# Optimization experiments

Hardware: AMD Instinct MI355X
Metric: run time of the kernel (lower is better)

The kernel has to match this reference:

```python
import jax, jax.numpy as jnp
import numpy as np

D, R, C = 4, 6, 32
P = 2 * R + 1          # 13 (both pixel patch and memory patch, since memory_patch_R == R)
N = P * P              # 169
DIL_INT = 15


def corr_sampler(f1, f2, p, dil):
    """SpatialCorrelationSampler(kernel_size=1, patch_size=p, dilation_patch=dil).
    out[b,i,j,y,x] = sum_c f1[b,c,y,x] * f2[b,c, y+(i-Rp)*dil, x+(j-Rp)*dil] (zero pad)."""
    Rp = (p - 1) // 2
    pad = Rp * dil
    b, c, h, w = f1.shape
    f2p = jnp.pad(f2, ((0, 0), (0, 0), (pad, pad), (pad, pad)))
    outs = [jnp.einsum('bchw,bchw->bhw', f1, f2p[:, :, i * dil:i * dil + h, j * dil:j * dil + w])
            for i in range(p) for j in range(p)]
    return jnp.stack(outs, 1).reshape(b, p, p, h, w)


def bilinear_gather(im, ys, xs):
    """Bilinear sample im [b,c,H,W] at float coords ys,xs [b,N,h,w]; zeros outside."""
    H, W = im.shape[2], im.shape[3]
    y0 = jnp.floor(ys)
    x0 = jnp.floor(xs)
    wy = ys - y0
    wx = xs - x0

    def g(yi, xi):
        valid = ((yi >= 0) & (yi < H) & (xi >= 0) & (xi < W)).astype(im.dtype)
        yc = jnp.clip(yi, 0, H - 1).astype(jnp.int32)
        xc = jnp.clip(xi, 0, W - 1).astype(jnp.int32)
        out = jax.vmap(lambda imb, yb, xb: imb[:, yb, xb])(im, yc, xc)  # [b,c,N,h,w]
        return out * valid[:, None]

    return (g(y0, x0) * ((1 - wy) * (1 - wx))[:, None]
            + g(y0, x0 + 1) * ((1 - wy) * wx)[:, None]
            + g(y0 + 1, x0) * (wy * (1 - wx))[:, None]
            + g(y0 + 1, x0 + 1) * (wy * wx)[:, None])


def deform_im2col(im, offset, p):
    """Deformable im2col: for each output pixel (y,x) and kernel pos (ky,kx),
    bilinearly sample im at (y+ky-Rp+off_y, x+kx-Rp+off_x). offset [...,0]=x, [...,1]=y.
    Returns [b,c,p*p,h,w]."""
    b, c, h, w = im.shape
    Rp = (p - 1) // 2
    ky, kx = jnp.meshgrid(jnp.arange(p) - Rp, jnp.arange(p) - Rp, indexing='ij')
    ky = ky.reshape(-1).astype(im.dtype)
    kx = kx.reshape(-1).astype(im.dtype)
    ys = (jnp.arange(h, dtype=im.dtype)[None, None, :, None]
          + ky[None, :, None, None] + offset[..., 1][:, None])  # [b,N,h,w]
    xs = (jnp.arange(w, dtype=im.dtype)[None, None, None, :]
          + kx[None, :, None, None] + offset[..., 0][:, None])
    return bilinear_gather(im, ys, xs)


def unfold_patches(x, p, pad):
    """F.unfold(kernel_size=p, padding=pad) -> [b,c,p*p,h,w]."""
    b, c, h, w = x.shape
    xp = jnp.pad(x, ((0, 0), (0, 0), (pad, pad), (pad, pad)))
    cols = [xp[:, :, i:i + h, j:j + w] for i in range(p) for j in range(p)]
    return jnp.stack(cols, 2)


def _forward(feats_r, feats_t, quantized_r, ref_index, current_ind):
    ri = np.asarray(ref_index)
    ci = int(current_ind)
    diffs = [ci - int(x) for x in ri]
    nsearch = sum(1 for d in diffs if d > DIL_INT)
    dirates = [min(4, d // DIL_INT + 1) for d in diffs if d > DIL_INT]
    nref = feats_r.shape[0]
    b, c, h, w = feats_t.shape

    # offset grid: _y,_x = meshgrid(ij) so grid[...,0]=x-offset, grid[...,1]=y-offset
    _y, _x = jnp.meshgrid(jnp.arange(-R, R + 1), jnp.arange(-R, R + 1), indexing='ij')
    grid = jnp.stack([_x, _y], -1).astype(feats_t.dtype)  # [P,P,2]

    corrs_pixel = []
    offset0 = []
    for s in range(nsearch):
        cc = corr_sampler(feats_t, feats_r[s], P, dirates[s])             # [b,P,P,h,w]
        soft = jax.nn.softmax(cc.reshape(b, N, h * w), axis=1).reshape(b, P, P, h, w)
        off = jnp.einsum('bijhw,ijd->bhwd', soft, grid) * dirates[s]      # [b,h,w,2]
        offset0.append(off)
        col0 = deform_im2col(feats_r[s], off, P)                          # [b,c,N,h,w]
        corrs_pixel.append(jnp.einsum('bchw,bcnhw->bnhw', feats_t, col0).reshape(b, N, h * w))
    for ind in range(nsearch, nref):
        corrs_pixel.append(corr_sampler(feats_t, feats_r[ind], P, 1).reshape(b, N, h * w))

    corr_pixel = jax.nn.softmax(jnp.concatenate(corrs_pixel, 1), axis=1)  # [b,nref*N,h*w]

    # prep: float + stride-D subsampling (C-channel input, so no one-hot branch)
    qr = [quantized_r[i][:, :, ::D, ::D] for i in range(nref)]            # [b,C,h,w]
    cols = [deform_im2col(qr[i], offset0[i], P).reshape(b, C, N, h * w) for i in range(nsearch)]
    cols += [unfold_patches(qr[i], P, R).reshape(b, C, N, h * w) for i in range(nsearch, nref)]
    image_uf = jnp.concatenate(cols, 2)                                   # [b,C,nref*N,h*w]

    out = jnp.einsum('bkl,bckl->bcl', corr_pixel, image_uf).reshape(b, C, h, w)
    return out


def setup_inputs() -> dict:
    key = jax.random.key(0)
    k1, k2, k3 = jax.random.split(key, 3)
    feats_r = jax.random.normal(k1, (3, 1, 64, 56, 56), jnp.float32) * 0.2
    feats_t = jax.random.normal(k2, (1, 64, 56, 56), jnp.float32) * 0.2
    quantized_r = jax.random.uniform(k3, (3, 1, 32, 224, 224), jnp.float32)
    return {
        'feats_r': feats_r,
        'feats_t': feats_t,
        'quantized_r': quantized_r,
        'ref_index': np.array([0, 30, 39], dtype=np.int64),
        'current_ind': 40,
    }


def reference(feats_r, feats_t, quantized_r, ref_index, current_ind):
    return _forward(feats_r, feats_t, quantized_r, ref_index, current_ind)
```

## Files before the change

kernel.cpp:

```cpp
#include <hip/hip_runtime.h>

#define HW    56
#define NPIX  3136
#define CH    64
#define CQ    32
#define PS    13
#define NPOS  169
#define GS    14
#define NG    196
#define G1    15
#define NG1   225

typedef __attribute__((ext_vector_type(8))) short short8;
typedef __attribute__((ext_vector_type(8))) ushort ushort8;
typedef __attribute__((ext_vector_type(4))) float f32x4;

__device__ inline ushort f2bf(float f) {
  unsigned u = __float_as_uint(f);
  return (ushort)((u + 0x7fffu + ((u >> 16) & 1u)) >> 16);
}
__device__ inline float bf2f(ushort u) {
  return __uint_as_float((unsigned)u << 16);
}
__device__ inline void wave_sync() {
  asm volatile("s_waitcnt lgkmcnt(0)" ::: "memory");
  __builtin_amdgcn_sched_barrier(0);
}

__global__ __launch_bounds__(256) void prep_all(
    const float* __restrict__ ft_in,
    const float* __restrict__ fr_in,
    const float* __restrict__ q_in,
    ushort* __restrict__ ft_out,
    ushort* __restrict__ fr_out,
    ushort* __restrict__ qout,
    float* __restrict__ zrow) {
  __shared__ float smem[CQ * (HW + 1)];
  int bid = blockIdx.x, tid = threadIdx.x;
  if (bid < 784) {
    if (bid == 0 && tid < 64) zrow[tid] = 0.f;
    int m = bid / 196, t = bid - m * 196;
    int row0 = (t / 98) * 32;
    int col0 = (t - (t / 98) * 98) * 32;
    const float* src = (m == 0) ? ft_in : fr_in + (size_t)(m - 1) * CH * NPIX;
    ushort* dst      = (m == 0) ? ft_out : fr_out + (size_t)(m - 1) * NPIX * CH;
    int ty = tid >> 3, tx4 = (tid & 7) * 4;
    f32x4 v = *(const f32x4*)&src[(size_t)(row0 + ty) * NPIX + col0 + tx4];
    *(f32x4*)&smem[ty * 33 + tx4] = v;
    __syncthreads();
    int px = tid >> 3, c4 = (tid & 7) * 4;
    ushort4 o;
    o.x = f2bf(smem[(c4 + 0) * 33 + px]);
    o.y = f2bf(smem[(c4 + 1) * 33 + px]);
    o.z = f2bf(smem[(c4 + 2) * 33 + px]);
    o.w = f2bf(smem[(c4 + 3) * 33 + px]);
    *(ushort4*)&dst[(size_t)(col0 + px) * CH + row0 + c4] = o;
  } else {
    int q = bid - 784;
    int r = q / HW, yy = q - r * HW;
    for (int idx = tid; idx < CQ * HW; idx += 256) {
      int c = idx / HW, xx = idx - c * HW;
      smem[c * (HW + 1) + xx] = q_in[((size_t)(r * CQ + c) * 224 + yy * 4) * 224 + xx * 4];
    }
    __syncthreads();
    for (int idx = tid; idx < CQ * HW; idx += 256) {
      int xx = idx >> 5, c = idx & 31;
      qout[(size_t)r * NPIX * CQ + (size_t)(yy * HW + xx) * CQ + c] = f2bf(smem[c * (HW + 1) + xx]);
    }
  }
}

__global__ __launch_bounds__(256, 4) void colorizer_main(
    const ushort* __restrict__ ftb,
    const ushort* __restrict__ frb,
    const ushort* __restrict__ qrb,
    const ushort* __restrict__ zrow,
    float* __restrict__ out)
{
  __shared__ float C1[1024];
  __shared__ float C2[1024];
  __shared__ int   pw[4 * 832];
  __shared__ float Sas[4];
  __shared__ float fqr0[128];
  __shared__ float red2[512];

  int tid = threadIdx.x;
  int wid = tid >> 6, lane = tid & 63;
  int mrow = lane & 15, klane = lane >> 4;

  int bx = blockIdx.x % 28, by = blockIdx.x / 28;
  int Y0 = by * 2, X0 = bx * 2;
  int dy = wid >> 1, dx = wid & 1;
  int y = Y0 + dy, x = X0 + dx;
  int pix = y * HW + x;

  int*   wb   = pw + wid * 832;
  float* e    = (float*)wb;
  float* D    = (float*)(wb + 176);
  float* wg   = (float*)(wb + 384);
  int*   offg = wb + 608;
  float* cc   = (float*)offg;

  if (lane < 16) offg[208 + lane] = -1;

  const ushort* frb0 = frb;
  const ushort* frb1 = frb + (size_t)NPIX * CH;
  const ushort* frb2 = frb + (size_t)2 * NPIX * CH;
  const ushort* qr0b = qrb;
  const ushort* qr1b = qrb + (size_t)NPIX * CQ;
  const ushort* qr2b = qrb + (size_t)2 * NPIX * CQ;

  const ushort* fb = ftb + (size_t)pix * CH;
  const ushort* plo = (mrow == 0) ? (fb + klane * 8) : zrow;
  const ushort* phi = (mrow == 0) ? (fb + 32 + klane * 8) : zrow;
  short8 b_lo = *(const short8*)plo;
  short8 b_hi = *(const short8*)phi;

  const ushort* fb4 = (mrow < 4)
      ? (ftb + (size_t)((Y0 + (mrow >> 1)) * HW + X0 + (mrow & 1)) * CH)
      : zrow;
  short8 b4_lo = *(const short8*)(fb4 + klane * 8);
  short8 b4_hi = *(const short8*)(fb4 + 32 + klane * 8);

#pragma unroll
  for (int k = 0; k < 8; ++k) {
    int j = wid + 4 * k;
    if (j < 30) {
      int r = (j >= 15);
      int t = j - r * 15;
      int g = t * 16 + mrow;
      int gy = g / G1, gx = g - gy * G1;
      int sy = Y0 - 6 + gy, sx = X0 - 6 + gx;
      bool v = (g < NG1) && ((unsigned)sy < HW) && ((unsigned)sx < HW);
      const ushort* base = r ? frb2 : frb1;
      const ushort* rb = v ? (base + (size_t)(sy * HW + sx) * CH) : zrow;
      short8 alo = *(const short8*)(rb + klane * 8);
      short8 ahi = *(const short8*)(rb + 32 + klane * 8);
      f32x4 acc = {0.f, 0.f, 0.f, 0.f};
      acc = __builtin_amdgcn_mfma_f32_16x16x32_bf16(alo, b4_lo, acc, 0, 0, 0);
      acc = __builtin_amdgcn_mfma_f32_16x16x32_bf16(ahi, b4_hi, acc, 0, 0, 0);
      int col = lane & 15;
      if (col < 4) {
        float* Cd = r ? C2 : C1;
        int row0 = t * 16 + (lane >> 4) * 4;
#pragma unroll
        for (int q = 0; q < 4; ++q) Cd[(row0 + q) * 4 + col] = acc[q];
      }
    }
  }
  __syncthreads();

#pragma unroll
  for (int g = 0; g < 11; ++g) {
    int d = g * 16 + mrow;
    int ii = d / PS, jj = d - ii * PS;
    int sy = y + (ii - 6) * 3, sx = x + (jj - 6) * 3;
    bool v = (d < NPOS) && ((unsigned)sy < HW) && ((unsigned)sx < HW);
    const ushort* rb = v ? (frb0 + (size_t)(sy * HW + sx) * CH) : zrow;
    short8 alo = *(const short8*)(rb + klane * 8);
    short8 ahi = *(const short8*)(rb + 32 + klane * 8);
    f32x4 acc = {0.f, 0.f, 0.f, 0.f};
    acc = __builtin_amdgcn_mfma_f32_16x16x32_bf16(alo, b_lo, acc, 0, 0, 0);
    acc = __builtin_amdgcn_mfma_f32_16x16x32_bf16(ahi, b_hi, acc, 0, 0, 0);
    if (mrow == 0) *(f32x4*)&cc[g * 16 + klane * 4] = acc;
  }
  wave_sync();

  float se = 0.f, sxe = 0.f, sye = 0.f;
#pragma unroll
  for (int k = 0; k < 3; ++k) {
    int id = lane + 64 * k;
    if (id < NPOS) {
      float ex = __expf(cc[id]);
      int pi = id / PS, pj = id - (id / PS) * PS;
      se += ex;
      sxe += ex * (float)(pj - 6);
      sye += ex * (float)(pi - 6);
    }
  }
#pragma unroll
  for (int o = 1; o < 64; o <<= 1) {
    se  += __shfl_xor(se, o);
    sxe += __shfl_xor(sxe, o);
    sye += __shfl_xor(sye, o);
  }
  float offx = 3.f * sxe / se;
  float offy = 3.f * sye / se;

  float fy0 = floorf(offy), fx0 = floorf(offx);
  int   iy0 = (int)fy0,     ix0 = (int)fx0;
  float wyf = offy - fy0,   wxf = offx - fx0;
  float w00 = (1.f - wyf) * (1.f - wxf), w01 = (1.f - wyf) * wxf;
  float w10 = wyf * (1.f - wxf),         w11 = wyf * wxf;

#pragma unroll
  for (int g = 0; g < 13; ++g) {
    int d = g * 16 + mrow;
    int a = d / GS, bq = d - a * GS;
    int sy = y + iy0 + a - 6, sx = x + ix0 + bq - 6;
    bool vA = (d < NG) && ((unsigned)sy < HW) && ((unsigned)sx < HW);
    int roA = sy * HW + sx;
    const ushort* rbA = vA ? (frb0 + (size_t)roA * CH) : zrow;
    short8 aAlo = *(const short8*)(rbA + klane * 8);
    short8 aAhi = *(const short8*)(rbA + 32 + klane * 8);
    f32x4 accA = {0.f, 0.f, 0.f, 0.f};
    accA = __builtin_amdgcn_mfma_f32_16x16x32_bf16(aAlo, b_lo, accA, 0, 0, 0);
    accA = __builtin_amdgcn_mfma_f32_16x16x32_bf16(aAhi, b_hi, accA, 0, 0, 0);
    if (klane == 0) offg[d] = vA ? roA : -1;
    if (mrow == 0) *(f32x4*)&D[g * 16 + klane * 4] = accA;
  }
  wave_sync();

  float ps = 0.f;
#pragma unroll
  for (int k = 0; k < 3; ++k) {
    int id = lane + 64 * k;
    if (id < NPOS) {
      int pi = id / PS, pj = id - (id / PS) * PS;
      float c0 = w00 * D[pi * GS + pj]       + w01 * D[pi * GS + pj + 1]
               + w10 * D[(pi + 1) * GS + pj] + w11 * D[(pi + 1) * GS + pj + 1];
      float ex = __expf(c0);
      e[id] = ex;
      ps += ex;
    } else if (id < 176) {
      e[id] = 0.f;
    }
    if (id < NPOS) {
      int ii = id / PS, jj = id - (id / PS) * PS;
      int g = (ii + dy) * G1 + (jj + dx);
      ps += __expf(C1[g * 4 + wid]) + __expf(C2[g * 4 + wid]);
    }
  }
#pragma unroll
  for (int o = 1; o < 64; o <<= 1) ps += __shfl_xor(ps, o);
  if (lane == 0) Sas[wid] = ps;
  wave_sync();

#pragma unroll
  for (int k = 0; k < 4; ++k) {
    int t = lane + 64 * k;
    if (t < 224) {
      float acc = 0.f;
      if (t < NG) {
        int a = t / GS, bq2 = t - (t / GS) * GS;
        if (a < PS && bq2 < PS) acc += w00 * e[a * PS + bq2];
        if (a < PS && bq2 >= 1) acc += w01 * e[a * PS + bq2 - 1];
        if (a >= 1 && bq2 < PS) acc += w10 * e[(a - 1) * PS + bq2];
        if (a >= 1 && bq2 >= 1) acc += w11 * e[(a - 1) * PS + bq2 - 1];
      }
      wg[t] = acc;
    }
  }
  wave_sync();

  int slot = lane >> 2, ln4 = lane & 3;
  float acc8[8];
#pragma unroll
  for (int c = 0; c < 8; ++c) acc8[c] = 0.f;
#pragma unroll
  for (int k = 0; k < 14; ++k) {
    int d = slot + k * 16;
    int ro = offg[d];
    if (ro >= 0) {
      float w = wg[d];
      ushort8 u = *(const ushort8*)(qr0b + (size_t)ro * CQ + ln4 * 8);
#pragma unroll
      for (int c = 0; c < 8; ++c) acc8[c] = fmaf(w, bf2f(u[c]), acc8[c]);
    }
  }
#pragma unroll
  for (int o = 4; o <= 32; o <<= 1)
#pragma unroll
    for (int c = 0; c < 8; ++c) acc8[c] += __shfl_xor(acc8[c], o);
  if (lane < 4) {
#pragma unroll
    for (int c = 0; c < 8; ++c) fqr0[wid * 32 + lane * 8 + c] = acc8[c];
  }
  __syncthreads();

#pragma unroll
  for (int t = 0; t < 8; ++t) {
    int idx = tid + t * 256;
    int ref = idx >> 10;
    int ix = idx & 1023;
    int g = ix >> 2, p = ix & 3;
    int gy = g / G1, gx = g - gy * G1;
    int ii = gy - (p >> 1), jj = gx - (p & 1);
    bool win = (g < NG1) && ((unsigned)ii < PS) && ((unsigned)jj < PS);
    float* Cd = ref ? C2 : C1;
    float val = Cd[ix];
    Cd[ix] = win ? __expf(val) : 0.f;
  }
  __syncthreads();

  int q8 = tid & 7, s = tid >> 3;
  float a12[4][4];
#pragma unroll
  for (int p = 0; p < 4; ++p)
#pragma unroll
    for (int c = 0; c < 4; ++c) a12[p][c] = 0.f;
#pragma unroll
  for (int i = 0; i < 8; ++i) {
    int g = s + 32 * i;
    if (g < NG1) {
      int gy = g / G1, gx = g - gy * G1;
      int sy = Y0 - 6 + gy, sx = X0 - 6 + gx;
      if (((unsigned)sy < HW) && ((unsigned)sx < HW)) {
        size_t ro = (size_t)(sy * HW + sx) * CQ + q8 * 4;
        ushort4 u1 = *(const ushort4*)(qr1b + ro);
        ushort4 u2 = *(const ushort4*)(qr2b + ro);
        f32x4 w1 = *(f32x4*)&C1[g * 4];
        f32x4 w2 = *(f32x4*)&C2[g * 4];
        float q1[4] = {bf2f(u1.x), bf2f(u1.y), bf2f(u1.z), bf2f(u1.w)};
        float q2[4] = {bf2f(u2.x), bf2f(u2.y), bf2f(u2.z), bf2f(u2.w)};
#pragma unroll
        for (int p = 0; p < 4; ++p)
#pragma unroll
          for (int c = 0; c < 4; ++c)
            a12[p][c] += w1[p] * q1[c] + w2[p] * q2[c];
      }
    }
  }
#pragma unroll
  for (int o = 8; o <= 32; o <<= 1)
#pragma unroll
    for (int p = 0; p < 4; ++p)
#pragma unroll
      for (int c = 0; c < 4; ++c)
        a12[p][c] += __shfl_xor(a12[p][c], o);
  if (lane < 8) {
#pragma unroll
    for (int p = 0; p < 4; ++p)
#pragma unroll
      for (int c = 0; c < 4; ++c)
        red2[wid * 128 + lane * 16 + p * 4 + c] = a12[p][c];
  }
  __syncthreads();

  if (tid < 128) {
    int p = tid >> 5, c = tid & 31;
    float tot = fqr0[p * 32 + c];
#pragma unroll
    for (int w = 0; w < 4; ++w)
      tot += red2[w * 128 + (c >> 2) * 16 + p * 4 + (c & 3)];
    int pidx = (Y0 + (p >> 1)) * HW + X0 + (p & 1);
    out[(size_t)c * NPIX + pidx] = tot / Sas[p];
  }
}

extern "C" void kernel_launch(void* const* d_in, const int* in_sizes, int n_in,
                              void* d_out, int out_size, void* d_ws, size_t ws_size,
                              hipStream_t stream) {
  const float* feats_r     = (const float*)d_in[0];
  const float* feats_t     = (const float*)d_in[1];
  const float* quantized_r = (const float*)d_in[2];

  ushort* ftb = (ushort*)d_ws;
  ushort* frb = ftb + 200704;
  ushort* qrb = frb + 602112;
  float*  zro = (float*)(qrb + 301056);

  prep_all<<<952, 256, 0, stream>>>(feats_t, feats_r, quantized_r,
                                    ftb, frb, qrb, zro);
  colorizer_main<<<784, 256, 0, stream>>>(ftb, frb, qrb, (const ushort*)zro,
                                          (float*)d_out);
}
```

Measured before the change: 44.13 us.

## Split colorizer into separate search and fixed-reference blocks with combine kernel

The monolithic per-tile kernel is split so that even blocks compute the two fixed-window references and odd blocks compute the deformable search reference. Each writes partial numerators and softmax denominators to workspace, and a new combine kernel sums them and normalises. Shared memory per block shrinks and the launch-bounds occupancy hint rises from 4 to 6, with twice as many blocks, to expose more parallelism. The cost is an extra kernel launch and a global round trip for the partial results.

```diff
diff --git a/kernel.cpp b/kernel.cpp
--- a/kernel.cpp
+++ b/kernel.cpp
@@ -70,38 +70,30 @@
   }
 }
 
-__global__ __launch_bounds__(256, 4) void colorizer_main(
+__global__ __launch_bounds__(256, 6) void colorizer_split(
     const ushort* __restrict__ ftb,
     const ushort* __restrict__ frb,
     const ushort* __restrict__ qrb,
     const ushort* __restrict__ zrow,
-    float* __restrict__ out)
+    float* __restrict__ pX,
+    float* __restrict__ pY,
+    float* __restrict__ SX,
+    float* __restrict__ SY)
 {
-  __shared__ float C1[1024];
-  __shared__ float C2[1024];
-  __shared__ int   pw[4 * 832];
-  __shared__ float Sas[4];
-  __shared__ float fqr0[128];
-  __shared__ float red2[512];
+  __shared__ int smem[4 * 832];
 
   int tid = threadIdx.x;
   int wid = tid >> 6, lane = tid & 63;
   int mrow = lane & 15, klane = lane >> 4;
 
-  int bx = blockIdx.x % 28, by = blockIdx.x / 28;
+  int bid = blockIdx.x;
+  int tile = bid >> 1;
+  bool isX = (bid & 1) == 0;
+  int bx = tile % 28, by = tile / 28;
   int Y0 = by * 2, X0 = bx * 2;
   int dy = wid >> 1, dx = wid & 1;
   int y = Y0 + dy, x = X0 + dx;
   int pix = y * HW + x;
-
-  int*   wb   = pw + wid * 832;
-  float* e    = (float*)wb;
-  float* D    = (float*)(wb + 176);
-  float* wg   = (float*)(wb + 384);
-  int*   offg = wb + 608;
-  float* cc   = (float*)offg;
-
-  if (lane < 16) offg[208 + lane] = -1;
 
   const ushort* frb0 = frb;
   const ushort* frb1 = frb + (size_t)NPIX * CH;
@@ -110,241 +102,289 @@
   const ushort* qr1b = qrb + (size_t)NPIX * CQ;
   const ushort* qr2b = qrb + (size_t)2 * NPIX * CQ;
 
-  const ushort* fb = ftb + (size_t)pix * CH;
-  const ushort* plo = (mrow == 0) ? (fb + klane * 8) : zrow;
-  const ushort* phi = (mrow == 0) ? (fb + 32 + klane * 8) : zrow;
-  short8 b_lo = *(const short8*)plo;
-  short8 b_hi = *(const short8*)phi;
-
-  const ushort* fb4 = (mrow < 4)
-      ? (ftb + (size_t)((Y0 + (mrow >> 1)) * HW + X0 + (mrow & 1)) * CH)
-      : zrow;
-  short8 b4_lo = *(const short8*)(fb4 + klane * 8);
-  short8 b4_hi = *(const short8*)(fb4 + 32 + klane * 8);
-
-#pragma unroll
-  for (int k = 0; k < 8; ++k) {
-    int j = wid + 4 * k;
-    if (j < 30) {
-      int r = (j >= 15);
-      int t = j - r * 15;
-      int g = t * 16 + mrow;
+  if (isX) {
+    float* C1   = (float*)smem;
+    float* C2   = (float*)smem + 1024;
+    float* red2 = (float*)smem + 2048;
+
+    const ushort* fb4 = (mrow < 4)
+        ? (ftb + (size_t)((Y0 + (mrow >> 1)) * HW + X0 + (mrow & 1)) * CH)
+        : zrow;
+    short8 b4_lo = *(const short8*)(fb4 + klane * 8);
+    short8 b4_hi = *(const short8*)(fb4 + 32 + klane * 8);
+
+#pragma unroll
+    for (int k = 0; k < 8; ++k) {
+      int j = wid + 4 * k;
+      if (j < 30) {
+        int r = (j >= 15);
+        int t = j - r * 15;
+        int g = t * 16 + mrow;
+        int gy = g / G1, gx = g - gy * G1;
+        int sy = Y0 - 6 + gy, sx = X0 - 6 + gx;
+        bool v = (g < NG1) && ((unsigned)sy < HW) && ((unsigned)sx < HW);
+        const ushort* base = r ? frb2 : frb1;
+        const ushort* rb = v ? (base + (size_t)(sy * HW + sx) * CH) : zrow;
+        short8 alo = *(const short8*)(rb + klane * 8);
+        short8 ahi = *(const short8*)(rb + 32 + klane * 8);
+        f32x4 acc = {0.f, 0.f, 0.f, 0.f};
+        acc = __builtin_amdgcn_mfma_f32_16x16x32_bf16(alo, b4_lo, acc, 0, 0, 0);
+        acc = __builtin_amdgcn_mfma_f32_16x16x32_bf16(ahi, b4_hi, acc, 0, 0, 0);
+        int col = lane & 15;
+        if (col < 4) {
+          float* Cd = r ? C2 : C1;
+          int row0 = t * 16 + (lane >> 4) * 4;
+#pragma unroll
+          for (int q = 0; q < 4; ++q) Cd[(row0 + q) * 4 + col] = acc[q];
+        }
+      }
+    }
+    __syncthreads();
+
+#pragma unroll
+    for (int t = 0; t < 8; ++t) {
+      int idx = tid + t * 256;
+      int ref = idx >> 10;
+      int ix = idx & 1023;
+      int g = ix >> 2, p = ix & 3;
       int gy = g / G1, gx = g - gy * G1;
-      int sy = Y0 - 6 + gy, sx = X0 - 6 + gx;
-      bool v = (g < NG1) && ((unsigned)sy < HW) && ((unsigned)sx < HW);
-      const ushort* base = r ? frb2 : frb1;
-      const ushort* rb = v ? (base + (size_t)(sy * HW + sx) * CH) : zrow;
+      int ii = gy - (p >> 1), jj = gx - (p & 1);
+      bool win = (g < NG1) && ((unsigned)ii < PS) && ((unsigned)jj < PS);
+      float* Cd = ref ? C2 : C1;
+      float val = Cd[ix];
+      Cd[ix] = win ? __expf(val) : 0.f;
+    }
+    __syncthreads();
+
+    float ps = 0.f;
+#pragma unroll
+    for (int k = 0; k < 3; ++k) {
+      int id = lane + 64 * k;
+      if (id < NPOS) {
+        int ii = id / PS, jj = id - (id / PS) * PS;
+        int g = (ii + dy) * G1 + (jj + dx);
+        ps += C1[g * 4 + wid] + C2[g * 4 + wid];
+      }
+    }
+#pragma unroll
+    for (int o = 1; o < 64; o <<= 1) ps += __shfl_xor(ps, o);
+    if (lane == 0) SX[pix] = ps;
+
+    int q8 = tid & 7, s = tid >> 3;
+    float a12[4][4];
+#pragma unroll
+    for (int p = 0; p < 4; ++p)
+#pragma unroll
+      for (int c = 0; c < 4; ++c) a12[p][c] = 0.f;
+#pragma unroll
+    for (int i = 0; i < 8; ++i) {
+      int g = s + 32 * i;
+      if (g < NG1) {
+        int gy = g / G1, gx = g - gy * G1;
+        int sy = Y0 - 6 + gy, sx = X0 - 6 + gx;
+        if (((unsigned)sy < HW) && ((unsigned)sx < HW)) {
+          size_t ro = (size_t)(sy * HW + sx) * CQ + q8 * 4;
+          ushort4 u1 = *(const ushort4*)(qr1b + ro);
+          ushort4 u2 = *(const ushort4*)(qr2b + ro);
+          f32x4 w1 = *(f32x4*)&C1[g * 4];
+          f32x4 w2 = *(f32x4*)&C2[g * 4];
+          float q1[4] = {bf2f(u1.x), bf2f(u1.y), bf2f(u1.z), bf2f(u1.w)};
+          float q2[4] = {bf2f(u2.x), bf2f(u2.y), bf2f(u2.z), bf2f(u2.w)};
+#pragma unroll
+          for (int p = 0; p < 4; ++p)
+#pragma unroll
+            for (int c = 0; c < 4; ++c)
+              a12[p][c] += w1[p] * q1[c] + w2[p] * q2[c];
+        }
+      }
+    }
+#pragma unroll
+    for (int o = 8; o <= 32; o <<= 1)
+#pragma unroll
+      for (int p = 0; p < 4; ++p)
+#pragma unroll
+        for (int c = 0; c < 4; ++c)
+          a12[p][c] += __shfl_xor(a12[p][c], o);
+    if (lane < 8) {
+#pragma unroll
+      for (int p = 0; p < 4; ++p)
+#pragma unroll
+        for (int c = 0; c < 4; ++c)
+          red2[wid * 128 + lane * 16 + p * 4 + c] = a12[p][c];
+    }
+    __syncthreads();
+
+    if (tid < 128) {
+      int p = tid >> 5, c = tid & 31;
+      float tot = 0.f;
+#pragma unroll
+      for (int w = 0; w < 4; ++w)
+        tot += red2[w * 128 + (c >> 2) * 16 + p * 4 + (c & 3)];
+      int pidx = (Y0 + (p >> 1)) * HW + X0 + (p & 1);
+      pX[(size_t)pidx * 32 + c] = tot;
+    }
+  } else {
+    int* wb = smem + wid * 832;
+    float* e  = (float*)wb;
+    float* D  = (float*)(wb + 176);
+    float* wg = (float*)(wb + 384);
+    int* offg = wb + 608;
+    float* cc = (float*)offg;
+    if (lane < 16) offg[208 + lane] = -1;
+
+    const ushort* fb = ftb + (size_t)pix * CH;
+    const ushort* plo = (mrow == 0) ? (fb + klane * 8) : zrow;
+    const ushort* phi = (mrow == 0) ? (fb + 32 + klane * 8) : zrow;
+    short8 b_lo = *(const short8*)plo;
+    short8 b_hi = *(const short8*)phi;
+
+#pragma unroll
+    for (int g = 0; g < 11; ++g) {
+      int d = g * 16 + mrow;
+      int ii = d / PS, jj = d - ii * PS;
+      int sy = y + (ii - 6) * 3, sx = x + (jj - 6) * 3;
+      bool v = (d < NPOS) && ((unsigned)sy < HW) && ((unsigned)sx < HW);
+      const ushort* rb = v ? (frb0 + (size_t)(sy * HW + sx) * CH) : zrow;
       short8 alo = *(const short8*)(rb + klane * 8);
       short8 ahi = *(const short8*)(rb + 32 + klane * 8);
       f32x4 acc = {0.f, 0.f, 0.f, 0.f};
-      acc = __builtin_amdgcn_mfma_f32_16x16x32_bf16(alo, b4_lo, acc, 0, 0, 0);
-      acc = __builtin_amdgcn_mfma_f32_16x16x32_bf16(ahi, b4_hi, acc, 0, 0, 0);
-      int col = lane & 15;
-      if (col < 4) {
-        float* Cd = r ? C2 : C1;
-        int row0 = t * 16 + (lane >> 4) * 4;
-#pragma unroll
-        for (int q = 0; q < 4; ++q) Cd[(row0 + q) * 4 + col] = acc[q];
-      }
-    }
+      acc = __builtin_amdgcn_mfma_f32_16x16x32_bf16(alo, b_lo, acc, 0, 0, 0);
+      acc = __builtin_amdgcn_mfma_f32_16x16x32_bf16(ahi, b_hi, acc, 0, 0, 0);
+      if (mrow == 0) *(f32x4*)&cc[g * 16 + klane * 4] = acc;
+    }
+    wave_sync();
+
+    float se = 0.f, sxe = 0.f, sye = 0.f;
+#pragma unroll
+    for (int k = 0; k < 3; ++k) {
+      int id = lane + 64 * k;
+      if (id < NPOS) {
+        float ex = __expf(cc[id]);
+        int pi = id / PS, pj = id - (id / PS) * PS;
+        se += ex;
+        sxe += ex * (float)(pj - 6);
+        sye += ex * (float)(pi - 6);
+      }
+    }
+#pragma unroll
+    for (int o = 1; o < 64; o <<= 1) {
+      se  += __shfl_xor(se, o);
+      sxe += __shfl_xor(sxe, o);
+      sye += __shfl_xor(sye, o);
+    }
+    float offx = 3.f * sxe / se;
+    float offy = 3.f * sye / se;
+
+    float fy0 = floorf(offy), fx0 = floorf(offx);
+    int   iy0 = (int)fy0,     ix0 = (int)fx0;
+    float wyf = offy - fy0,   wxf = offx - fx0;
+    float w00 = (1.f - wyf) * (1.f - wxf), w01 = (1.f - wyf) * wxf;
+    float w10 = wyf * (1.f - wxf),         w11 = wyf * wxf;
+
+#pragma unroll
+    for (int g = 0; g < 13; ++g) {
+      int d = g * 16 + mrow;
+      int a = d / GS, bq = d - a * GS;
+      int sy = y + iy0 + a - 6, sx = x + ix0 + bq - 6;
+      bool vA = (d < NG) && ((unsigned)sy < HW) && ((unsigned)sx < HW);
+      int roA = sy * HW + sx;
+      const ushort* rbA = vA ? (frb0 + (size_t)roA * CH) : zrow;
+      short8 aAlo = *(const short8*)(rbA + klane * 8);
+      short8 aAhi = *(const short8*)(rbA + 32 + klane * 8);
+      f32x4 accA = {0.f, 0.f, 0.f, 0.f};
+      accA = __builtin_amdgcn_mfma_f32_16x16x32_bf16(aAlo, b_lo, accA, 0, 0, 0);
+      accA = __builtin_amdgcn_mfma_f32_16x16x32_bf16(aAhi, b_hi, accA, 0, 0, 0);
+      if (klane == 0) offg[d] = vA ? roA : -1;
+      if (mrow == 0) *(f32x4*)&D[g * 16 + klane * 4] = accA;
+    }
+    wave_sync();
+
+    float ps = 0.f;
+#pragma unroll
+    for (int k = 0; k < 3; ++k) {
+      int id = lane + 64 * k;
+      if (id < NPOS) {
+        int pi = id / PS, pj = id - (id / PS) * PS;
+        float c0 = w00 * D[pi * GS + pj]       + w01 * D[pi * GS + pj + 1]
+                 + w10 * D[(pi + 1) * GS + pj] + w11 * D[(pi + 1) * GS + pj + 1];
+        float ex = __expf(c0);
+        e[id] = ex;
+        ps += ex;
+      } else if (id < 176) {
+        e[id] = 0.f;
+      }
+    }
+#pragma unroll
+    for (int o = 1; o < 64; o <<= 1) ps += __shfl_xor(ps, o);
+    wave_sync();
+
+#pragma unroll
+    for (int k = 0; k < 4; ++k) {
+      int t = lane + 64 * k;
+      if (t < 224) {
+        float acc = 0.f;
+        if (t < NG) {
+          int a = t / GS, b2 = t - (t / GS) * GS;
+          if (a < PS && b2 < PS) acc += w00 * e[a * PS + b2];
+          if (a < PS && b2 >= 1) acc += w01 * e[a * PS + b2 - 1];
+          if (a >= 1 && b2 < PS) acc += w10 * e[(a - 1) * PS + b2];
+          if (a >= 1 && b2 >= 1) acc += w11 * e[(a - 1) * PS + b2 - 1];
+        }
+        wg[t] = acc;
+      }
+    }
+    wave_sync();
+
+    int slot = lane >> 2, ln4 = lane & 3;
+    float acc8[8];
+#pragma unroll
+    for (int c = 0; c < 8; ++c) acc8[c] = 0.f;
+#pragma unroll
+    for (int k = 0; k < 14; ++k) {
+      int d = slot + k * 16;
+      int ro = offg[d];
+      if (ro >= 0) {
+        float w = wg[d];
+        ushort8 u = *(const ushort8*)(qr0b + (size_t)ro * CQ + ln4 * 8);
+#pragma unroll
+        for (int c = 0; c < 8; ++c) acc8[c] = fmaf(w, bf2f(u[c]), acc8[c]);
+      }
+    }
+#pragma unroll
+    for (int o = 4; o <= 32; o <<= 1)
+#pragma unroll
+      for (int c = 0; c < 8; ++c) acc8[c] += __shfl_xor(acc8[c], o);
+    if (lane < 4) {
+      f32x4 lo = {acc8[0], acc8[1], acc8[2], acc8[3]};
+      f32x4 hi = {acc8[4], acc8[5], acc8[6], acc8[7]};
+      *(f32x4*)&pY[(size_t)pix * 32 + lane * 8]     = lo;
+      *(f32x4*)&pY[(size_t)pix * 32 + lane * 8 + 4] = hi;
+    }
+    if (lane == 0) SY[pix] = ps;
   }
+}
+
+__global__ __launch_bounds__(256) void combine(
+    const float* __restrict__ pX, const float* __restrict__ pY,
+    const float* __restrict__ SX, const float* __restrict__ SY,
+    float* __restrict__ out) {
+  __shared__ float t[32][33];
+  __shared__ float inv[32];
+  int pix0 = blockIdx.x * 32;
+  int tid = threadIdx.x;
+#pragma unroll
+  for (int k = 0; k < 4; ++k) {
+    int idx = tid + 256 * k;
+    int p = idx >> 5, c = idx & 31;
+    t[p][c] = pX[(size_t)(pix0 + p) * 32 + c] + pY[(size_t)(pix0 + p) * 32 + c];
+  }
+  if (tid < 32) inv[tid] = 1.f / (SX[pix0 + tid] + SY[pix0 + tid]);
   __syncthreads();
-
-#pragma unroll
-  for (int g = 0; g < 11; ++g) {
-    int d = g * 16 + mrow;
-    int ii = d / PS, jj = d - ii * PS;
-    int sy = y + (ii - 6) * 3, sx = x + (jj - 6) * 3;
-    bool v = (d < NPOS) && ((unsigned)sy < HW) && ((unsigned)sx < HW);
-    const ushort* rb = v ? (frb0 + (size_t)(sy * HW + sx) * CH) : zrow;
-    short8 alo = *(const short8*)(rb + klane * 8);
-    short8 ahi = *(const short8*)(rb + 32 + klane * 8);
-    f32x4 acc = {0.f, 0.f, 0.f, 0.f};
-    acc = __builtin_amdgcn_mfma_f32_16x16x32_bf16(alo, b_lo, acc, 0, 0, 0);
-    acc = __builtin_amdgcn_mfma_f32_16x16x32_bf16(ahi, b_hi, acc, 0, 0, 0);
-    if (mrow == 0) *(f32x4*)&cc[g * 16 + klane * 4] = acc;
-  }
-  wave_sync();
-
-  float se = 0.f, sxe = 0.f, sye = 0.f;
-#pragma unroll
-  for (int k = 0; k < 3; ++k) {
-    int id = lane + 64 * k;
-    if (id < NPOS) {
-      float ex = __expf(cc[id]);
-      int pi = id / PS, pj = id - (id / PS) * PS;
-      se += ex;
-      sxe += ex * (float)(pj - 6);
-      sye += ex * (float)(pi - 6);
-    }
-  }
-#pragma unroll
-  for (int o = 1; o < 64; o <<= 1) {
-    se  += __shfl_xor(se, o);
-    sxe += __shfl_xor(sxe, o);
-    sye += __shfl_xor(sye, o);
-  }
-  float offx = 3.f * sxe / se;
-  float offy = 3.f * sye / se;
-
-  float fy0 = floorf(offy), fx0 = floorf(offx);
-  int   iy0 = (int)fy0,     ix0 = (int)fx0;
-  float wyf = offy - fy0,   wxf = offx - fx0;
-  float w00 = (1.f - wyf) * (1.f - wxf), w01 = (1.f - wyf) * wxf;
-  float w10 = wyf * (1.f - wxf),         w11 = wyf * wxf;
-
-#pragma unroll
-  for (int g = 0; g < 13; ++g) {
-    int d = g * 16 + mrow;
-    int a = d / GS, bq = d - a * GS;
-    int sy = y + iy0 + a - 6, sx = x + ix0 + bq - 6;
-    bool vA = (d < NG) && ((unsigned)sy < HW) && ((unsigned)sx < HW);
-    int roA = sy * HW + sx;
-    const ushort* rbA = vA ? (frb0 + (size_t)roA * CH) : zrow;
-    short8 aAlo = *(const short8*)(rbA + klane * 8);
-    short8 aAhi = *(const short8*)(rbA + 32 + klane * 8);
-    f32x4 accA = {0.f, 0.f, 0.f, 0.f};
-    accA = __builtin_amdgcn_mfma_f32_16x16x32_bf16(aAlo, b_lo, accA, 0, 0, 0);
-    accA = __builtin_amdgcn_mfma_f32_16x16x32_bf16(aAhi, b_hi, accA, 0, 0, 0);
-    if (klane == 0) offg[d] = vA ? roA : -1;
-    if (mrow == 0) *(f32x4*)&D[g * 16 + klane * 4] = accA;
-  }
-  wave_sync();
-
-  float ps = 0.f;
-#pragma unroll
-  for (int k = 0; k < 3; ++k) {
-    int id = lane + 64 * k;
-    if (id < NPOS) {
-      int pi = id / PS, pj = id - (id / PS) * PS;
-      float c0 = w00 * D[pi * GS + pj]       + w01 * D[pi * GS + pj + 1]
-               + w10 * D[(pi + 1) * GS + pj] + w11 * D[(pi + 1) * GS + pj + 1];
-      float ex = __expf(c0);
-      e[id] = ex;
-      ps += ex;
-    } else if (id < 176) {
-      e[id] = 0.f;
-    }
-    if (id < NPOS) {
-      int ii = id / PS, jj = id - (id / PS) * PS;
-      int g = (ii + dy) * G1 + (jj + dx);
-      ps += __expf(C1[g * 4 + wid]) + __expf(C2[g * 4 + wid]);
-    }
-  }
-#pragma unroll
-  for (int o = 1; o < 64; o <<= 1) ps += __shfl_xor(ps, o);
-  if (lane == 0) Sas[wid] = ps;
-  wave_sync();
-
 #pragma unroll
   for (int k = 0; k < 4; ++k) {
-    int t = lane + 64 * k;
-    if (t < 224) {
-      float acc = 0.f;
-      if (t < NG) {
-        int a = t / GS, bq2 = t - (t / GS) * GS;
-        if (a < PS && bq2 < PS) acc += w00 * e[a * PS + bq2];
-        if (a < PS && bq2 >= 1) acc += w01 * e[a * PS + bq2 - 1];
-        if (a >= 1 && bq2 < PS) acc += w10 * e[(a - 1) * PS + bq2];
-        if (a >= 1 && bq2 >= 1) acc += w11 * e[(a - 1) * PS + bq2 - 1];
-      }
-      wg[t] = acc;
-    }
-  }
-  wave_sync();
-
-  int slot = lane >> 2, ln4 = lane & 3;
-  float acc8[8];
-#pragma unroll
-  for (int c = 0; c < 8; ++c) acc8[c] = 0.f;
-#pragma unroll
-  for (int k = 0; k < 14; ++k) {
-    int d = slot + k * 16;
-    int ro = offg[d];
-    if (ro >= 0) {
-      float w = wg[d];
-      ushort8 u = *(const ushort8*)(qr0b + (size_t)ro * CQ + ln4 * 8);
-#pragma unroll
-      for (int c = 0; c < 8; ++c) acc8[c] = fmaf(w, bf2f(u[c]), acc8[c]);
-    }
-  }
-#pragma unroll
-  for (int o = 4; o <= 32; o <<= 1)
-#pragma unroll
-    for (int c = 0; c < 8; ++c) acc8[c] += __shfl_xor(acc8[c], o);
-  if (lane < 4) {
-#pragma unroll
-    for (int c = 0; c < 8; ++c) fqr0[wid * 32 + lane * 8 + c] = acc8[c];
-  }
-  __syncthreads();
-
-#pragma unroll
-  for (int t = 0; t < 8; ++t) {
-    int idx = tid + t * 256;
-    int ref = idx >> 10;
-    int ix = idx & 1023;
-    int g = ix >> 2, p = ix & 3;
-    int gy = g / G1, gx = g - gy * G1;
-    int ii = gy - (p >> 1), jj = gx - (p & 1);
-    bool win = (g < NG1) && ((unsigned)ii < PS) && ((unsigned)jj < PS);
-    float* Cd = ref ? C2 : C1;
-    float val = Cd[ix];
-    Cd[ix] = win ? __expf(val) : 0.f;
-  }
-  __syncthreads();
-
-  int q8 = tid & 7, s = tid >> 3;
-  float a12[4][4];
-#pragma unroll
-  for (int p = 0; p < 4; ++p)
-#pragma unroll
-    for (int c = 0; c < 4; ++c) a12[p][c] = 0.f;
-#pragma unroll
-  for (int i = 0; i < 8; ++i) {
-    int g = s + 32 * i;
-    if (g < NG1) {
-      int gy = g / G1, gx = g - gy * G1;
-      int sy = Y0 - 6 + gy, sx = X0 - 6 + gx;
-      if (((unsigned)sy < HW) && ((unsigned)sx < HW)) {
-        size_t ro = (size_t)(sy * HW + sx) * CQ + q8 * 4;
-        ushort4 u1 = *(const ushort4*)(qr1b + ro);
-        ushort4 u2 = *(const ushort4*)(qr2b + ro);
-        f32x4 w1 = *(f32x4*)&C1[g * 4];
-        f32x4 w2 = *(f32x4*)&C2[g * 4];
-        float q1[4] = {bf2f(u1.x), bf2f(u1.y), bf2f(u1.z), bf2f(u1.w)};
-        float q2[4] = {bf2f(u2.x), bf2f(u2.y), bf2f(u2.z), bf2f(u2.w)};
-#pragma unroll
-        for (int p = 0; p < 4; ++p)
-#pragma unroll
-          for (int c = 0; c < 4; ++c)
-            a12[p][c] += w1[p] * q1[c] + w2[p] * q2[c];
-      }
-    }
-  }
-#pragma unroll
-  for (int o = 8; o <= 32; o <<= 1)
-#pragma unroll
-    for (int p = 0; p < 4; ++p)
-#pragma unroll
-      for (int c = 0; c < 4; ++c)
-        a12[p][c] += __shfl_xor(a12[p][c], o);
-  if (lane < 8) {
-#pragma unroll
-    for (int p = 0; p < 4; ++p)
-#pragma unroll
-      for (int c = 0; c < 4; ++c)
-        red2[wid * 128 + lane * 16 + p * 4 + c] = a12[p][c];
-  }
-  __syncthreads();
-
-  if (tid < 128) {
-    int p = tid >> 5, c = tid & 31;
-    float tot = fqr0[p * 32 + c];
-#pragma unroll
-    for (int w = 0; w < 4; ++w)
-      tot += red2[w * 128 + (c >> 2) * 16 + p * 4 + (c & 3)];
-    int pidx = (Y0 + (p >> 1)) * HW + X0 + (p & 1);
-    out[(size_t)c * NPIX + pidx] = tot / Sas[p];
+    int idx = tid + 256 * k;
+    int c = idx >> 5, p = idx & 31;
+    out[(size_t)c * NPIX + pix0 + p] = t[p][c] * inv[p];
   }
 }
 
@@ -359,9 +399,14 @@
   ushort* frb = ftb + 200704;
   ushort* qrb = frb + 602112;
   float*  zro = (float*)(qrb + 301056);
+  float*  pX  = zro + 64;
+  float*  pY  = pX + 100352;
+  float*  SXp = pY + 100352;
+  float*  SYp = SXp + 3136;
 
   prep_all<<<952, 256, 0, stream>>>(feats_t, feats_r, quantized_r,
                                     ftb, frb, qrb, zro);
-  colorizer_main<<<784, 256, 0, stream>>>(ftb, frb, qrb, (const ushort*)zro,
-                                          (float*)d_out);
-}
+  colorizer_split<<<1568, 256, 0, stream>>>(ftb, frb, qrb, (const ushort*)zro,
+                                            pX, pY, SXp, SYp);
+  combine<<<98, 256, 0, stream>>>(pX, pY, SXp, SYp, (float*)d_out);
+}
```

New measurement: 51.59 us. 16.9% more time.
